# Optimization experiments

Hardware: AMD Instinct MI355X
Metric: run time of the kernel (lower is better)

Reference implementation:

```python
import jax, jax.numpy as jnp
import numpy as np

NUM_GRAPHS = 64


def gcn_conv(x, W, b, row, col, ew, n_nodes):
    # PyG GCNConv with edge weights: add self-loops (weight 1), symmetric norm.
    deg = jax.ops.segment_sum(ew, col, num_segments=n_nodes) + 1.0  # self-loop weight
    dis = jnp.where(deg > 0, jax.lax.rsqrt(deg), 0.0)
    norm = dis[row] * ew * dis[col]  # [E]
    xw = x @ W  # [N, H]
    # edge messages aggregated at target (col) + self-loop contribution dis_i^2 * xw_i
    agg = jnp.zeros_like(xw).at[col].add(norm[:, None] * xw[row])
    agg = agg + (dis * dis)[:, None] * xw
    return agg + b


def reference(x, edge_index, edge_attr, batch, W1, b1, W2, b2, actor_w, actor_b, critic_w, critic_b):
    n_nodes = x.shape[0]
    row, col = edge_index[0], edge_index[1]
    ew = jnp.abs(edge_attr)
    h = jax.nn.relu(gcn_conv(x, W1, b1, row, col, ew, n_nodes))
    # dropout p=0.1 is identity in eval mode
    h = jax.nn.relu(gcn_conv(h, W2, b2, row, col, ew, n_nodes))
    action_logits = (h @ actor_w + actor_b)[:, 0]  # [N]
    # global mean pool over graphs
    sums = jax.ops.segment_sum(h, batch, num_segments=NUM_GRAPHS)  # [G, H]
    counts = jax.ops.segment_sum(jnp.ones((n_nodes,), h.dtype), batch, num_segments=NUM_GRAPHS)
    graph_embed = sums / jnp.maximum(counts, 1.0)[:, None]
    value = graph_embed @ critic_w + critic_b  # [G, 1]
    return (action_logits, value)


def setup_inputs() -> dict:
    key = jax.random.key(0)
    ks = jax.random.split(key, 10)
    N, F, H, E = 100000, 128, 64, 1600000
    s = lambda fan: 1.0 / np.sqrt(fan)
    return {
        "x": jax.random.normal(ks[0], (N, F), jnp.float32),
        "edge_index": jax.random.randint(ks[1], (2, E), 0, N, jnp.int32),
        "edge_attr": jax.random.normal(ks[2], (E,), jnp.float32),
        "batch": jnp.sort(jax.random.randint(ks[3], (N,), 0, 64, jnp.int32)),
        "W1": jax.random.normal(ks[4], (F, H), jnp.float32) * s(F),
        "b1": jnp.zeros((H,), jnp.float32),
        "W2": jax.random.normal(ks[5], (H, H), jnp.float32) * s(H),
        "b2": jnp.zeros((H,), jnp.float32),
        "actor_w": jax.random.normal(ks[6], (H, 1), jnp.float32) * s(H),
        "actor_b": jnp.zeros((1,), jnp.float32),
        "critic_w": jax.random.normal(ks[7], (H, 1), jnp.float32) * s(H),
        "critic_b": jnp.zeros((1,), jnp.float32),
    }
```

## Files before the change

### kernel.cpp

```cpp
#include <hip/hip_runtime.h>
#include <hip/hip_fp16.h>


#define TB 256
#define BSH2 9
#define BW2 512
#define CHUNK 4096
#define NB1MAX 256
#define PAD 8

#define FMA_ROW(ar, xv)                                                        \
    ar.x = fmaf(xv.x, w0.x, ar.x); ar.y = fmaf(xv.x, w0.y, ar.y);              \
    ar.z = fmaf(xv.x, w0.z, ar.z); ar.w = fmaf(xv.x, w0.w, ar.w);              \
    ar.x = fmaf(xv.y, w1.x, ar.x); ar.y = fmaf(xv.y, w1.y, ar.y);              \
    ar.z = fmaf(xv.y, w1.z, ar.z); ar.w = fmaf(xv.y, w1.w, ar.w);              \
    ar.x = fmaf(xv.z, w2.x, ar.x); ar.y = fmaf(xv.z, w2.y, ar.y);              \
    ar.z = fmaf(xv.z, w2.z, ar.z); ar.w = fmaf(xv.z, w2.w, ar.w);              \
    ar.x = fmaf(xv.w, w3.x, ar.x); ar.y = fmaf(xv.w, w3.y, ar.y);              \
    ar.z = fmaf(xv.w, w3.z, ar.z); ar.w = fmaf(xv.w, w3.w, ar.w);

__global__ __launch_bounds__(256) void buildA_gemm1_k(
        const int* __restrict__ col, const int* __restrict__ row,
        const float* __restrict__ ea, int* __restrict__ gCur,
        uint2* __restrict__ recA, int E, int CAPB, int NB1, int NBA,
        const float* __restrict__ X, const float* __restrict__ W,
        __half* __restrict__ Y, int N) {
    __shared__ __align__(16) char smem[64 * 132 * 4];
    const int t = threadIdx.x;
    if (blockIdx.x < NBA) {
        int* hist = (int*)smem;
        int* base = hist + NB1MAX;
        int* cur  = base + NB1MAX;
        int e0 = blockIdx.x * CHUNK;
        if (t < NB1MAX) { hist[t] = 0; cur[t] = 0; }
        __syncthreads();
        for (int i = t; i < CHUNK; i += 256) {
            int e = e0 + i;
            if (e < E) atomicAdd(&hist[col[e] >> BSH2], 1);
        }
        __syncthreads();
        if (t < NB1) base[t] = atomicAdd(&gCur[t], hist[t]);
        __syncthreads();
        for (int i = t; i < CHUNK; i += 256) {
            int e = e0 + i;
            if (e >= E) continue;
            int c = col[e];
            int b = c >> BSH2;
            int pos = base[b] + atomicAdd(&cur[b], 1);
            if (pos < CAPB)
                recA[(size_t)b * CAPB + pos] =
                    make_uint2(((unsigned)(c & (BW2 - 1)) << 17) | (unsigned)row[e],
                               __float_as_uint(fabsf(ea[e])));
        }
    } else {
        const int K = 128, KS = 132;
        float* xs = (float*)smem;
        const int row0 = (blockIdx.x - NBA) * 64;
        float4* xs4 = reinterpret_cast<float4*>(xs);
        const float4* X4 = reinterpret_cast<const float4*>(X + (size_t)row0 * K);
        for (int idx = t; idx < 64 * (K / 4); idx += 256) {
            int rl = idx >> 5, k4 = idx & 31;
            int r = row0 + rl;
            xs4[rl * 33 + k4] = (r < N) ? X4[idx] : float4{0.f, 0.f, 0.f, 0.f};
        }
        __syncthreads();
        const int cg = t & 15;
        const int rg = t >> 4;
        const float4* W4 = reinterpret_cast<const float4*>(W);
        const float4* xr0 = reinterpret_cast<const float4*>(xs + (rg * 4 + 0) * KS);
        const float4* xr1 = reinterpret_cast<const float4*>(xs + (rg * 4 + 1) * KS);
        const float4* xr2 = reinterpret_cast<const float4*>(xs + (rg * 4 + 2) * KS);
        const float4* xr3 = reinterpret_cast<const float4*>(xs + (rg * 4 + 3) * KS);
        float4 a0 = {0.f, 0.f, 0.f, 0.f}, a1 = a0, a2 = a0, a3 = a0;
#pragma unroll 2
        for (int k4 = 0; k4 < K / 4; ++k4) {
            float4 x0 = xr0[k4], x1 = xr1[k4], x2 = xr2[k4], x3 = xr3[k4];
            float4 w0 = W4[(k4 * 4 + 0) * 16 + cg];
            float4 w1 = W4[(k4 * 4 + 1) * 16 + cg];
            float4 w2 = W4[(k4 * 4 + 2) * 16 + cg];
            float4 w3 = W4[(k4 * 4 + 3) * 16 + cg];
            FMA_ROW(a0, x0)
            FMA_ROW(a1, x1)
            FMA_ROW(a2, x2)
            FMA_ROW(a3, x3)
        }
        int r = row0 + rg * 4;
        __half2* yp0 = reinterpret_cast<__half2*>(Y + (size_t)r * 64 + cg * 4);
        if (r < N) {
            yp0[0] = __float22half2_rn(make_float2(a0.x, a0.y));
            yp0[1] = __float22half2_rn(make_float2(a0.z, a0.w));
        }
        if (r + 1 < N) {
            __half2* yp = yp0 + 32;
            yp[0] = __float22half2_rn(make_float2(a1.x, a1.y));
            yp[1] = __float22half2_rn(make_float2(a1.z, a1.w));
        }
        if (r + 2 < N) {
            __half2* yp = yp0 + 64;
            yp[0] = __float22half2_rn(make_float2(a2.x, a2.y));
            yp[1] = __float22half2_rn(make_float2(a2.z, a2.w));
        }
        if (r + 3 < N) {
            __half2* yp = yp0 + 96;
            yp[0] = __float22half2_rn(make_float2(a3.x, a3.y));
            yp[1] = __float22half2_rn(make_float2(a3.z, a3.w));
        }
    }
}

__global__ __launch_bounds__(256) void passB_k(const int* __restrict__ gCur,
                                               const uint2* __restrict__ recA,
                                               uint2* __restrict__ rec,
                                               int* __restrict__ ptr,
                                               int* __restrict__ cnt,
                                               float* __restrict__ dis,
                                               int N, int CAPB) {
    __shared__ int hist[BW2], excl[BW2], cur[BW2];
    __shared__ float sumL[BW2];
    __shared__ int part[256];
    int b = blockIdx.x, t = threadIdx.x;
    int nrec = min(gCur[b], CAPB);
    for (int i = t; i < BW2; i += 256) { hist[i] = 0; cur[i] = 0; sumL[i] = 0.f; }
    __syncthreads();
    const uint2* ra = recA + (size_t)b * CAPB;
    for (int i = t; i < nrec; i += 256) {
        uint2 r = ra[i];
        int lc = r.x >> 17;
        atomicAdd(&hist[lc], 1);
        atomicAdd(&sumL[lc], __uint_as_float(r.y));
    }
    __syncthreads();
    int p0 = (hist[t * 2] + PAD - 1) & ~(PAD - 1);
    int p1 = (hist[t * 2 + 1] + PAD - 1) & ~(PAD - 1);
    int s = p0 + p1;
    part[t] = s;
    __syncthreads();
    for (int d = 1; d < 256; d <<= 1) {
        int v = (t >= d) ? part[t - d] : 0;
        __syncthreads();
        part[t] += v;
        __syncthreads();
    }
    int poff = t ? part[t - 1] : 0;
    excl[t * 2] = poff;
    excl[t * 2 + 1] = poff + p0;
    __syncthreads();
    for (int i = t; i < nrec; i += 256) {
        uint2 r = ra[i];
        int lc = r.x >> 17;
        int pos = atomicAdd(&cur[lc], 1);
        rec[(size_t)b * CAPB + excl[lc] + pos] = make_uint2(r.x & 0x1FFFFu, r.y);
    }
    __syncthreads();
    int c0 = b << BSH2;
    for (int i = t; i < BW2; i += 256) {
        int node = c0 + i;
        int hv = hist[i];
        int pc = (hv + PAD - 1) & ~(PAD - 1);
        for (int j = hv; j < pc; ++j)
            rec[(size_t)b * CAPB + excl[i] + j] = make_uint2(0u, 0u);
        if (node < N) {
            ptr[node] = b * CAPB + excl[i];
            cnt[node] = pc;
            dis[node] = rsqrtf(sumL[i] + 1.0f);
        }
    }
}

__global__ __launch_bounds__(256) void gemm2_k(const __half* __restrict__ X,
                                               const float* __restrict__ W,
                                               __half* __restrict__ Y, int N) {
    const int K = 64, KS = 68;
    __shared__ float xs[64 * KS];
    const int tid = threadIdx.x;
    const int row0 = blockIdx.x * 64;
    float4* xs4 = reinterpret_cast<float4*>(xs);
    const __half2* X2 = reinterpret_cast<const __half2*>(X + (size_t)row0 * K);
    for (int idx = tid; idx < 64 * (K / 4); idx += 256) {
        int rl = idx >> 4, k4 = idx & 15;
        int r = row0 + rl;
        if (r < N) {
            float2 fa = __half22float2(X2[2 * idx]);
            float2 fb = __half22float2(X2[2 * idx + 1]);
            xs4[rl * 17 + k4] = float4{fa.x, fa.y, fb.x, fb.y};
        } else xs4[rl * 17 + k4] = float4{0.f, 0.f, 0.f, 0.f};
    }
    __syncthreads();
    const int cg = tid & 15;
    const int rg = tid >> 4;
    const float4* W4 = reinterpret_cast<const float4*>(W);
    const float4* xr0 = reinterpret_cast<const float4*>(xs + (rg * 4 + 0) * KS);
    const float4* xr1 = reinterpret_cast<const float4*>(xs + (rg * 4 + 1) * KS);
    const float4* xr2 = reinterpret_cast<const float4*>(xs + (rg * 4 + 2) * KS);
    const float4* xr3 = reinterpret_cast<const float4*>(xs + (rg * 4 + 3) * KS);
    float4 a0 = {0.f, 0.f, 0.f, 0.f}, a1 = a0, a2 = a0, a3 = a0;
#pragma unroll 2
    for (int k4 = 0; k4 < K / 4; ++k4) {
        float4 x0 = xr0[k4], x1 = xr1[k4], x2 = xr2[k4], x3 = xr3[k4];
        float4 w0 = W4[(k4 * 4 + 0) * 16 + cg];
        float4 w1 = W4[(k4 * 4 + 1) * 16 + cg];
        float4 w2 = W4[(k4 * 4 + 2) * 16 + cg];
        float4 w3 = W4[(k4 * 4 + 3) * 16 + cg];
        FMA_ROW(a0, x0)
        FMA_ROW(a1, x1)
        FMA_ROW(a2, x2)
        FMA_ROW(a3, x3)
    }
    int r = row0 + rg * 4;
    __half2* yp0 = reinterpret_cast<__half2*>(Y + (size_t)r * 64 + cg * 4);
    if (r < N) {
        yp0[0] = __float22half2_rn(make_float2(a0.x, a0.y));
        yp0[1] = __float22half2_rn(make_float2(a0.z, a0.w));
    }
    if (r + 1 < N) {
        __half2* yp = yp0 + 32;
        yp[0] = __float22half2_rn(make_float2(a1.x, a1.y));
        yp[1] = __float22half2_rn(make_float2(a1.z, a1.w));
    }
    if (r + 2 < N) {
        __half2* yp = yp0 + 64;
        yp[0] = __float22half2_rn(make_float2(a2.x, a2.y));
        yp[1] = __float22half2_rn(make_float2(a2.z, a2.w));
    }
    if (r + 3 < N) {
        __half2* yp = yp0 + 96;
        yp[0] = __float22half2_rn(make_float2(a3.x, a3.y));
        yp[1] = __float22half2_rn(make_float2(a3.z, a3.w));
    }
}

template <bool WITH_LOGITS>
__global__ __launch_bounds__(256) void agg_fin_k(const int* __restrict__ ptr,
                                                 const int* __restrict__ cnt,
                                                 const uint2* __restrict__ rec,
                                                 const float* __restrict__ dis,
                                                 const __half2* __restrict__ xw2,
                                                 const float* __restrict__ bias,
                                                 __half2* __restrict__ hout,
                                                 const float* __restrict__ aw,
                                                 const float* __restrict__ ab,
                                                 float* __restrict__ logits, int N) {
    int n = blockIdx.x * 4 + (threadIdx.x >> 6);
    if (n >= N) return;
    int lane = threadIdx.x & 63;
    int half_id = lane >> 5;
    int fl = lane & 31;
    int base = ptr[n], num = cnt[n];
    float ax = 0.f, ay = 0.f;
    for (int k0 = 0; k0 < num; k0 += 64) {
        int rem = min(num - k0, 64);
        int r = 0; float w = 0.f;
        if (lane < rem) {
            uint2 rv = rec[(size_t)base + k0 + lane];
            r = (int)rv.x;
            w = __uint_as_float(rv.y) * dis[r];
        }
#pragma unroll 2
        for (int k = 0; k < rem; k += 8) {
            int i0 = k + half_id;
            int   ra0 = __shfl(r, i0),     ra1 = __shfl(r, i0 + 2);
            int   ra2 = __shfl(r, i0 + 4), ra3 = __shfl(r, i0 + 6);
            float wa0 = __shfl(w, i0),     wa1 = __shfl(w, i0 + 2);
            float wa2 = __shfl(w, i0 + 4), wa3 = __shfl(w, i0 + 6);
            __half2 v0 = xw2[(size_t)ra0 * 32 + fl];
            __half2 v1 = xw2[(size_t)ra1 * 32 + fl];
            __half2 v2 = xw2[(size_t)ra2 * 32 + fl];
            __half2 v3 = xw2[(size_t)ra3 * 32 + fl];
            float2 f;
            f = __half22float2(v0); ax = fmaf(wa0, f.x, ax); ay = fmaf(wa0, f.y, ay);
            f = __half22float2(v1); ax = fmaf(wa1, f.x, ax); ay = fmaf(wa1, f.y, ay);
            f = __half22float2(v2); ax = fmaf(wa2, f.x, ax); ay = fmaf(wa2, f.y, ay);
            f = __half22float2(v3); ax = fmaf(wa3, f.x, ax); ay = fmaf(wa3, f.y, ay);
        }
    }
    ax += __shfl(ax, lane ^ 32);
    ay += __shfl(ay, lane ^ 32);
    if (half_id == 0) {
        float d = dis[n];
        float2 xs = __half22float2(xw2[(size_t)n * 32 + fl]);
        float2 bb = reinterpret_cast<const float2*>(bias)[fl];
        float2 out;
        out.x = fmaxf(fmaf(d, fmaf(d, xs.x, ax), bb.x), 0.0f);
        out.y = fmaxf(fmaf(d, fmaf(d, xs.y, ay), bb.y), 0.0f);
        hout[(size_t)n * 32 + fl] = __float22half2_rn(out);
        if constexpr (WITH_LOGITS) {
            float2 awv = reinterpret_cast<const float2*>(aw)[fl];
            float lg = out.x * awv.x + out.y * awv.y;
            lg += __shfl(lg, lane ^ 1);
            lg += __shfl(lg, lane ^ 2);
            lg += __shfl(lg, lane ^ 4);
            lg += __shfl(lg, lane ^ 8);
            lg += __shfl(lg, lane ^ 16);
            if (lane == 0) logits[n] = lg + ab[0];
        }
    }
}

__global__ __launch_bounds__(256) void pool_k(const __half2* __restrict__ h2,
                                              const int* __restrict__ batch,
                                              float* __restrict__ sums,
                                              float* __restrict__ counts,
                                              int N, int C) {
    int wave = blockIdx.x * 4 + (threadIdx.x >> 6);
    int lane = threadIdx.x & 63;
    int start = wave * C;
    if (start >= N) return;
    if (lane >= 32) return;
    int end = min(start + C, N);
    int fl = lane;
    int cur = batch[start];
    float accx = 0.f, accy = 0.f;
    int cntv = 0;
    for (int i = start; i < end; ++i) {
        float2 v = __half22float2(h2[(size_t)i * 32 + fl]);
        int g = batch[i];
        if (g != cur) {
            atomicAdd(&sums[cur * 64 + 2 * fl], accx);
            atomicAdd(&sums[cur * 64 + 2 * fl + 1], accy);
            if (fl == 0) atomicAdd(&counts[cur], (float)cntv);
            accx = 0.f; accy = 0.f; cntv = 0; cur = g;
        }
        accx += v.x; accy += v.y; ++cntv;
    }
    atomicAdd(&sums[cur * 64 + 2 * fl], accx);
    atomicAdd(&sums[cur * 64 + 2 * fl + 1], accy);
    if (fl == 0) atomicAdd(&counts[cur], (float)cntv);
}

__global__ void value_k(const float* __restrict__ sums, const float* __restrict__ counts,
                        const float* __restrict__ cw, const float* __restrict__ cb,
                        float* __restrict__ val) {
    int g = blockIdx.x;
    int lane = threadIdx.x;
    float cntv = fmaxf(counts[g], 1.0f);
    float p = (sums[g * 64 + lane] / cntv) * cw[lane];
    for (int off = 32; off; off >>= 1) p += __shfl_down(p, off);
    if (lane == 0) val[g] = p + cb[0];
}

extern "C" void kernel_launch(void* const* d_in, const int* in_sizes, int n_in,
                              void* d_out, int out_size, void* d_ws, size_t ws_size,
                              hipStream_t stream) {
    const float* x     = (const float*)d_in[0];
    const int*   ei    = (const int*)d_in[1];
    const float* ea    = (const float*)d_in[2];
    const int*   batch = (const int*)d_in[3];
    const float* W1    = (const float*)d_in[4];
    const float* b1    = (const float*)d_in[5];
    const float* W2    = (const float*)d_in[6];
    const float* b2    = (const float*)d_in[7];
    const float* aw    = (const float*)d_in[8];
    const float* ab    = (const float*)d_in[9];
    const float* cw    = (const float*)d_in[10];
    const float* cb    = (const float*)d_in[11];

    const int N = in_sizes[3];
    const int E = in_sizes[2];
    const int H = 64, G = 64;
    const int* row = ei;
    const int* col = ei + E;

    const int NB1  = (N + BW2 - 1) >> BSH2;
    const int CAPB = (((E / NB1) * 3 / 2 + 512) + 1) & ~1;
    const int NBA  = (E + CHUNK - 1) / CHUNK;
    const int NG1  = (N + 63) / 64;

    float*  sums   = (float*)d_ws;
    float*  counts = sums + G * H;
    int*    gCur   = (int*)(counts + G);
    float*  dis    = (float*)(gCur + NB1MAX);
    uint2*  recA   = (uint2*)(dis + N);
    uint2*  rec    = recA + (size_t)NB1 * CAPB;
    int*    ptr    = (int*)(rec + (size_t)NB1 * CAPB);
    int*    cnt    = ptr + N;
    __half* xwh    = (__half*)(cnt + N);
    __half* hbuf   = xwh + (size_t)N * H;

    float* logits = (float*)d_out;
    float* value  = logits + N;

    hipMemsetAsync(sums, 0, (size_t)(G * H + G + NB1MAX) * 4, stream);

    buildA_gemm1_k<<<NBA + NG1, 256, 0, stream>>>(col, row, ea, gCur, recA,
                                                  E, CAPB, NB1, NBA,
                                                  x, W1, xwh, N);
    passB_k<<<NB1, 256, 0, stream>>>(gCur, recA, rec, ptr, cnt, dis, N, CAPB);

    agg_fin_k<false><<<(N + 3) / 4, 256, 0, stream>>>(ptr, cnt, rec, dis,
        (const __half2*)xwh, b1, (__half2*)hbuf, nullptr, nullptr, nullptr, N);

    gemm2_k<<<(N + 63) / 64, 256, 0, stream>>>(hbuf, W2, xwh, N);
    agg_fin_k<true><<<(N + 3) / 4, 256, 0, stream>>>(ptr, cnt, rec, dis,
        (const __half2*)xwh, b2, (__half2*)hbuf, aw, ab, logits, N);

    const int WAVES = 4096;
    const int C = (N + WAVES - 1) / WAVES;
    pool_k<<<WAVES / 4, 256, 0, stream>>>((const __half2*)hbuf, batch, sums, counts, N, C);
    value_k<<<G, 64, 0, stream>>>(sums, counts, cw, cb, value);
}
```

Baseline: 235.2 us.

## Double-buffer GEMM1 X tiles with async global-to-LDS loads

The first-layer GEMM no longer stages the whole 64x128 X tile into padded shared memory before computing. It now streams X in four K-slices of 32, using direct global-to-LDS loads into two buffers so the next slice loads while the current one is multiplied. Shared memory per block shrinks from about 33 KB to 16 KB, which may allow more resident blocks. The cost is extra barriers per slice and unpadded 32-float LDS rows, which can cause bank conflicts; correctness also relies on the compiler waiting for the async loads before each barrier.

```diff
diff --git a/kernel.cpp b/kernel.cpp
--- a/kernel.cpp
+++ b/kernel.cpp
@@ -19,16 +19,19 @@
     ar.x = fmaf(xv.w, w3.x, ar.x); ar.y = fmaf(xv.w, w3.y, ar.y);              \
     ar.z = fmaf(xv.w, w3.z, ar.z); ar.w = fmaf(xv.w, w3.w, ar.w);
 
+typedef const __attribute__((address_space(1))) unsigned int* gptr_t;
+typedef __attribute__((address_space(3))) unsigned int* lptr_t;
+
 __global__ __launch_bounds__(256) void buildA_gemm1_k(
         const int* __restrict__ col, const int* __restrict__ row,
         const float* __restrict__ ea, int* __restrict__ gCur,
         uint2* __restrict__ recA, int E, int CAPB, int NB1, int NBA,
         const float* __restrict__ X, const float* __restrict__ W,
         __half* __restrict__ Y, int N) {
-    __shared__ __align__(16) char smem[64 * 132 * 4];
+    __shared__ __align__(16) float xs[2 * 64 * 32];
     const int t = threadIdx.x;
     if (blockIdx.x < NBA) {
-        int* hist = (int*)smem;
+        int* hist = (int*)xs;
         int* base = hist + NB1MAX;
         int* cur  = base + NB1MAX;
         int e0 = blockIdx.x * CHUNK;
@@ -53,36 +56,49 @@
                                __float_as_uint(fabsf(ea[e])));
         }
     } else {
-        const int K = 128, KS = 132;
-        float* xs = (float*)smem;
+        const int K = 128;
         const int row0 = (blockIdx.x - NBA) * 64;
-        float4* xs4 = reinterpret_cast<float4*>(xs);
-        const float4* X4 = reinterpret_cast<const float4*>(X + (size_t)row0 * K);
-        for (int idx = t; idx < 64 * (K / 4); idx += 256) {
-            int rl = idx >> 5, k4 = idx & 31;
-            int r = row0 + rl;
-            xs4[rl * 33 + k4] = (r < N) ? X4[idx] : float4{0.f, 0.f, 0.f, 0.f};
-        }
-        __syncthreads();
         const int cg = t & 15;
         const int rg = t >> 4;
         const float4* W4 = reinterpret_cast<const float4*>(W);
-        const float4* xr0 = reinterpret_cast<const float4*>(xs + (rg * 4 + 0) * KS);
-        const float4* xr1 = reinterpret_cast<const float4*>(xs + (rg * 4 + 1) * KS);
-        const float4* xr2 = reinterpret_cast<const float4*>(xs + (rg * 4 + 2) * KS);
-        const float4* xr3 = reinterpret_cast<const float4*>(xs + (rg * 4 + 3) * KS);
-        float4 a0 = {0.f, 0.f, 0.f, 0.f}, a1 = a0, a2 = a0, a3 = a0;
-#pragma unroll 2
-        for (int k4 = 0; k4 < K / 4; ++k4) {
-            float4 x0 = xr0[k4], x1 = xr1[k4], x2 = xr2[k4], x3 = xr3[k4];
-            float4 w0 = W4[(k4 * 4 + 0) * 16 + cg];
-            float4 w1 = W4[(k4 * 4 + 1) * 16 + cg];
-            float4 w2 = W4[(k4 * 4 + 2) * 16 + cg];
-            float4 w3 = W4[(k4 * 4 + 3) * 16 + cg];
-            FMA_ROW(a0, x0)
-            FMA_ROW(a1, x1)
-            FMA_ROW(a2, x2)
-            FMA_ROW(a3, x3)
+        const int rrA = t >> 3,          k4A = t & 7;
+        const int rrB = (t + 256) >> 3,  k4B = t & 7;
+        const int grA = min(row0 + rrA, N - 1);
+        const int grB = min(row0 + rrB, N - 1);
+#define G1_ISSUE(kt, buf)                                                      \
+    {                                                                          \
+        const float* gA = X + (size_t)grA * K + (kt) + k4A * 4;                \
+        const float* gB = X + (size_t)grB * K + (kt) + k4B * 4;                \
+        __builtin_amdgcn_global_load_lds((gptr_t)gA,                           \
+            (lptr_t)(xs + (buf) * 2048 + t * 4), 16, 0, 0);                    \
+        __builtin_amdgcn_global_load_lds((gptr_t)gB,                           \
+            (lptr_t)(xs + (buf) * 2048 + (t + 256) * 4), 16, 0, 0);            \
+    }
+        const float4 z4 = {0.f, 0.f, 0.f, 0.f};
+        float4 a0 = z4, a1 = z4, a2 = z4, a3 = z4;
+        G1_ISSUE(0, 0)
+        __syncthreads();
+        for (int kt = 0; kt < 4; ++kt) {
+            if (kt < 3) G1_ISSUE((kt + 1) * 32, (kt + 1) & 1)
+            const float* xb = xs + (kt & 1) * 2048;
+            const float4* xr0 = reinterpret_cast<const float4*>(xb + (rg * 4 + 0) * 32);
+            const float4* xr1 = reinterpret_cast<const float4*>(xb + (rg * 4 + 1) * 32);
+            const float4* xr2 = reinterpret_cast<const float4*>(xb + (rg * 4 + 2) * 32);
+            const float4* xr3 = reinterpret_cast<const float4*>(xb + (rg * 4 + 3) * 32);
+#pragma unroll
+            for (int k4 = 0; k4 < 8; ++k4) {
+                float4 x0 = xr0[k4], x1 = xr1[k4], x2 = xr2[k4], x3 = xr3[k4];
+                int kk = kt * 32 + k4 * 4;
+                float4 w0 = W4[(kk + 0) * 16 + cg];
+                float4 w1 = W4[(kk + 1) * 16 + cg];
+                float4 w2 = W4[(kk + 2) * 16 + cg];
+                float4 w3 = W4[(kk + 3) * 16 + cg];
+                FMA_ROW(a0, x0)
+                FMA_ROW(a1, x1)
+                FMA_ROW(a2, x2)
+                FMA_ROW(a3, x3)
+            }
+            __syncthreads();
         }
         int r = row0 + rg * 4;
         __half2* yp0 = reinterpret_cast<__half2*>(Y + (size_t)r * 64 + cg * 4);
@@ -105,6 +121,7 @@
             yp[0] = __float22half2_rn(make_float2(a3.x, a3.y));
             yp[1] = __float22half2_rn(make_float2(a3.z, a3.w));
         }
+#undef G1_ISSUE
     }
 }
 
@@ -277,11 +294,11 @@
     ay += __shfl(ay, lane ^ 32);
     if (half_id == 0) {
         float d = dis[n];
-        float2 xs = __half22float2(xw2[(size_t)n * 32 + fl]);
+        float2 xsv = __half22float2(xw2[(size_t)n * 32 + fl]);
         float2 bb = reinterpret_cast<const float2*>(bias)[fl];
         float2 out;
-        out.x = fmaxf(fmaf(d, fmaf(d, xs.x, ax), bb.x), 0.0f);
-        out.y = fmaxf(fmaf(d, fmaf(d, xs.y, ay), bb.y), 0.0f);
+        out.x = fmaxf(fmaf(d, fmaf(d, xsv.x, ax), bb.x), 0.0f);
+        out.y = fmaxf(fmaf(d, fmaf(d, xsv.y, ay), bb.y), 0.0f);
         hout[(size_t)n * 32 + fl] = __float22half2_rn(out);
         if constexpr (WITH_LOGITS) {
             float2 awv = reinterpret_cast<const float2*>(aw)[fl];
```

New measurement: 233.7 us (median of 2 runs). Within noise of the previous version (-0.6%).
